# Performance work log

Measured on AMD Instinct MI355X. Metric: run time of the kernel, lower is better.

Reference implementation:

```python
import jax, jax.numpy as jnp
import numpy as np

N_NODES = 100000
N_EDGES = 600000
D_FEAT = 128
HID = 128


def setup_inputs() -> dict:
    key = jax.random.key(0)
    ks = jax.random.split(key, 8)
    zi = jax.random.normal(ks[0], (N_NODES, D_FEAT), dtype=jnp.float32)
    zj = jax.random.normal(ks[1], (N_NODES, D_FEAT), dtype=jnp.float32)
    src = jax.random.randint(ks[2], (N_EDGES,), 0, N_NODES, dtype=jnp.int64 if jax.config.jax_enable_x64 else jnp.int32)
    dst = jax.random.randint(ks[3], (N_EDGES,), 0, N_NODES, dtype=jnp.int64 if jax.config.jax_enable_x64 else jnp.int32)
    W1 = jax.random.normal(ks[4], (2 * D_FEAT, HID), dtype=jnp.float32) * (1.0 / np.sqrt(2 * D_FEAT))
    b1 = jnp.zeros((HID,), dtype=jnp.float32)
    W3 = jax.random.normal(ks[5], (HID, 1), dtype=jnp.float32) * (1.0 / np.sqrt(HID))
    b3 = jnp.zeros((1,), dtype=jnp.float32)
    return {"zi": zi, "zj": zj, "src": src, "dst": dst,
            "W1": W1, "b1": b1, "W3": W3, "b3": b3}


def reference(zi, zj, src, dst, W1, b1, W3, b3):
    # Irregular gather: per-edge src/dst node features, then concat -> [E, 2*d]
    hi = zi[src]              # [E, d]
    hj = zj[dst]              # [E, d]
    raw = jnp.concatenate([hi, hj], axis=1)  # [E, 2d]
    # LR_Classification with n_layers=2: only linear_1 and linear_3 run
    # (the linear_2 loop executes n_layers-2 = 0 times); dropout is identity (eval).
    hid = jax.nn.relu(raw @ W1 + b1)          # [E, HID]
    logit = hid @ W3 + b3                     # [E, 1]
    return jax.nn.sigmoid(logit)
```

## Files before the change

kernel.cpp:

```cpp
#include <hip/hip_runtime.h>
#include <hip/hip_bf16.h>

typedef __attribute__((ext_vector_type(8))) short short8;
typedef __attribute__((ext_vector_type(4))) float f32x4;
typedef __attribute__((ext_vector_type(4))) unsigned int u32x4;
typedef __attribute__((ext_vector_type(2))) unsigned int u32x2;

#define DFEAT 128
#define LDW 136

__device__ __forceinline__ unsigned short f2bf(float f) {
    unsigned int u = __float_as_uint(f);
    u += 0x7FFFu + ((u >> 16) & 1u);
    return (unsigned short)(u >> 16);
}
__device__ __forceinline__ unsigned int cvt2(float lo, float hi) {
    unsigned int r;
    asm("v_cvt_pk_bf16_f32 %0, %1, %2" : "=v"(r) : "v"(lo), "v"(hi));
    return r;
}
__device__ __forceinline__ float bf2f(unsigned int bits) {
    return __uint_as_float(bits << 16);
}

__global__ __launch_bounds__(256) void node_gemm(
    const float* __restrict__ zi, const float* __restrict__ zj,
    const float* __restrict__ W1, const float* __restrict__ b1,
    unsigned short* __restrict__ Aout, unsigned short* __restrict__ Bout,
    int nN)
{
    __shared__ unsigned short Wt[128][LDW];
    __shared__ float bias_lds[128];
    const int table = blockIdx.y;
    const float* __restrict__ z = table ? zj : zi;
    unsigned short* __restrict__ outp = table ? Bout : Aout;

    for (int idx = threadIdx.x; idx < 128 * 128; idx += 256) {
        int c = idx & 127, k = idx >> 7;
        Wt[c][k] = f2bf(W1[(size_t)(table * 128 + k) * DFEAT + c]);
    }
    if (threadIdx.x < 128) bias_lds[threadIdx.x] = table ? 0.f : b1[threadIdx.x];
    __syncthreads();

    const int lane = threadIdx.x & 63;
    const int l15  = lane & 15;
    const int kg   = lane >> 4;
    int wv = blockIdx.x * 4 + (threadIdx.x >> 6);
    int nw = gridDim.x * 4;
    int nStrips = (nN + 15) >> 4;

    float4 cur[8];
    int s = wv;
    if (s < nStrips) {
        int row = s * 16 + l15;
        const float* zr = z + (size_t)(row < nN ? row : nN - 1) * DFEAT + kg * 8;
#pragma unroll
        for (int kk = 0; kk < 4; ++kk) {
            cur[2 * kk]     = *(const float4*)(zr + kk * 32);
            cur[2 * kk + 1] = *(const float4*)(zr + kk * 32 + 4);
        }
    }

    while (s < nStrips) {
        short8 bf[4];
#pragma unroll
        for (int kk = 0; kk < 4; ++kk) {
            union { unsigned int u[4]; short8 s8; } cv;
            cv.u[0] = cvt2(cur[2 * kk].x,     cur[2 * kk].y);
            cv.u[1] = cvt2(cur[2 * kk].z,     cur[2 * kk].w);
            cv.u[2] = cvt2(cur[2 * kk + 1].x, cur[2 * kk + 1].y);
            cv.u[3] = cvt2(cur[2 * kk + 1].z, cur[2 * kk + 1].w);
            bf[kk] = cv.s8;
        }

        int snext = s + nw;
        if (snext < nStrips) {
            int row = snext * 16 + l15;
            const float* zr = z + (size_t)(row < nN ? row : nN - 1) * DFEAT + kg * 8;
#pragma unroll
            for (int kk = 0; kk < 4; ++kk) {
                cur[2 * kk]     = *(const float4*)(zr + kk * 32);
                cur[2 * kk + 1] = *(const float4*)(zr + kk * 32 + 4);
            }
        }

        int row = s * 16 + l15;
        unsigned short* op = outp + (size_t)row * DFEAT + kg * 4;
#pragma unroll
        for (int h = 0; h < 2; ++h) {
            f32x4 acc[4];
#pragma unroll
            for (int ci = 0; ci < 4; ++ci)
                acc[ci] = *(const f32x4*)&bias_lds[(h * 4 + ci) * 16 + kg * 4];
#pragma unroll
            for (int kk = 0; kk < 4; ++kk) {
#pragma unroll
                for (int ci = 0; ci < 4; ++ci) {
                    short8 a = *(const short8*)&Wt[(h * 4 + ci) * 16 + l15][kk * 32 + kg * 8];
                    acc[ci] = __builtin_amdgcn_mfma_f32_16x16x32_bf16(a, bf[kk], acc[ci], 0, 0, 0);
                }
            }
            if (row < nN) {
#pragma unroll
                for (int ci = 0; ci < 4; ++ci) {
                    u32x2 v;
                    v[0] = cvt2(acc[ci][0], acc[ci][1]);
                    v[1] = cvt2(acc[ci][2], acc[ci][3]);
                    *(u32x2*)(op + (h * 4 + ci) * 16) = v;
                }
            }
        }
        s = snext;
    }
}

__global__ __launch_bounds__(256) void edge_kernel(
    const unsigned short* __restrict__ A, const unsigned short* __restrict__ B,
    const int* __restrict__ src, const int* __restrict__ dst,
    const float* __restrict__ W3, const float* __restrict__ b3,
    float* __restrict__ out, int nE)
{
    const int lane = threadIdx.x & 63;
    const int sub  = lane & 15;
    const int grp  = lane >> 4;

    float w3v[8];
#pragma unroll
    for (int j = 0; j < 8; ++j) w3v[j] = W3[sub * 8 + j];
    const float bb = b3[0];

    int wv = blockIdx.x * 4 + (threadIdx.x >> 6);
    int nw = gridDim.x * 4;

    for (int base = wv * 8; base < nE; base += nw * 8) {
        int e0 = base + grp;
        int e1 = base + 4 + grp;
        bool v0 = e0 < nE, v1 = e1 < nE;
        int s0 = v0 ? src[e0] : 0, d0 = v0 ? dst[e0] : 0;
        int s1 = v1 ? src[e1] : 0, d1 = v1 ? dst[e1] : 0;

        const u32x4* pa0 = (const u32x4*)(A + (size_t)s0 * DFEAT + sub * 8);
        const u32x4* pb0 = (const u32x4*)(B + (size_t)d0 * DFEAT + sub * 8);
        const u32x4* pa1 = (const u32x4*)(A + (size_t)s1 * DFEAT + sub * 8);
        const u32x4* pb1 = (const u32x4*)(B + (size_t)d1 * DFEAT + sub * 8);
        u32x4 av0 = *pa0, bv0 = *pb0;
        u32x4 av1 = *pa1, bv1 = *pb1;

        float p0 = 0.f, p1 = 0.f;
#pragma unroll
        for (int w = 0; w < 4; ++w) {
            float x0 = fmaxf(bf2f(av0[w] & 0xFFFFu) + bf2f(bv0[w] & 0xFFFFu), 0.f);
            float x1 = fmaxf(bf2f(av0[w] >> 16)     + bf2f(bv0[w] >> 16),     0.f);
            p0 = fmaf(x0, w3v[w * 2], p0);
            p0 = fmaf(x1, w3v[w * 2 + 1], p0);
            float y0 = fmaxf(bf2f(av1[w] & 0xFFFFu) + bf2f(bv1[w] & 0xFFFFu), 0.f);
            float y1 = fmaxf(bf2f(av1[w] >> 16)     + bf2f(bv1[w] >> 16),     0.f);
            p1 = fmaf(y0, w3v[w * 2], p1);
            p1 = fmaf(y1, w3v[w * 2 + 1], p1);
        }
#pragma unroll
        for (int off = 8; off > 0; off >>= 1) {
            p0 += __shfl_xor(p0, off, 64);
            p1 += __shfl_xor(p1, off, 64);
        }
        if (sub == 0) {
            if (v0) out[e0] = 1.f / (1.f + __expf(-(p0 + bb)));
            if (v1) out[e1] = 1.f / (1.f + __expf(-(p1 + bb)));
        }
    }
}

__global__ __launch_bounds__(256) void fallback_kernel(
    const float* __restrict__ zi, const float* __restrict__ zj,
    const int* __restrict__ src, const int* __restrict__ dst,
    const float* __restrict__ W1, const float* __restrict__ b1,
    const float* __restrict__ W3, const float* __restrict__ b3,
    float* __restrict__ out, int nE)
{
    int e = blockIdx.x * blockDim.x + threadIdx.x;
    if (e >= nE) return;
    const float* a = zi + (size_t)src[e] * DFEAT;
    const float* b = zj + (size_t)dst[e] * DFEAT;
    float logit = b3[0];
    for (int h = 0; h < 128; ++h) {
        float acc = b1[h];
        for (int k = 0; k < 128; ++k) acc = fmaf(a[k], W1[(size_t)k * 128 + h], acc);
        for (int k = 0; k < 128; ++k) acc = fmaf(b[k], W1[(size_t)(128 + k) * 128 + h], acc);
        if (acc > 0.f) logit = fmaf(acc, W3[h], logit);
    }
    out[e] = 1.f / (1.f + __expf(-logit));
}

extern "C" void kernel_launch(void* const* d_in, const int* in_sizes, int n_in,
                              void* d_out, int out_size, void* d_ws, size_t ws_size,
                              hipStream_t stream) {
    const float* zi = (const float*)d_in[0];
    const float* zj = (const float*)d_in[1];
    const int*  src = (const int*)d_in[2];
    const int*  dst = (const int*)d_in[3];
    const float* W1 = (const float*)d_in[4];
    const float* b1 = (const float*)d_in[5];
    const float* W3 = (const float*)d_in[6];
    const float* b3 = (const float*)d_in[7];
    float* out = (float*)d_out;

    int nN = in_sizes[0] / DFEAT;
    int nE = in_sizes[2];
    size_t abytes = (size_t)nN * DFEAT * sizeof(unsigned short);

    if (ws_size >= 2 * abytes) {
        unsigned short* A = (unsigned short*)d_ws;
        unsigned short* B = A + (size_t)nN * DFEAT;
        dim3 g1(512, 2, 1);
        node_gemm<<<g1, 256, 0, stream>>>(zi, zj, W1, b1, A, B, nN);
        edge_kernel<<<2048, 256, 0, stream>>>(A, B, src, dst, W3, b3, out, nE);
    } else {
        fallback_kernel<<<(nE + 255) / 256, 256, 0, stream>>>(
            zi, zj, src, dst, W1, b1, W3, b3, out, nE);
    }
}
```

Baseline: 80.56 us.

## Double-buffer loads two iterations ahead in node GEMM and edge gather kernels

Both kernels now use two register buffers and issue the loads for iteration s+2 while computing iteration s. In the node GEMM this covers the strip loads; in the edge kernel it covers the index fetch and the gathered bf16 rows. Scheduling barriers keep the prefetch loads ahead of the compute. The edge grid also drops from 2048 to 1875 blocks, so each wave gets a whole number of 8-edge chunks. This hides more gather latency in exchange for higher register pressure, which may reduce occupancy.

```diff
diff --git a/kernel.cpp b/kernel.cpp
--- a/kernel.cpp
+++ b/kernel.cpp
@@ -21,6 +21,17 @@
 }
 __device__ __forceinline__ float bf2f(unsigned int bits) {
     return __uint_as_float(bits << 16);
+}
+
+__device__ __forceinline__ void load_strip(float4 (&buf)[8], const float* __restrict__ z,
+                                           int ss, int nN, int l15, int kg) {
+    int row = ss * 16 + l15;
+    const float* zr = z + (size_t)(row < nN ? row : nN - 1) * DFEAT + kg * 8;
+#pragma unroll
+    for (int kk = 0; kk < 4; ++kk) {
+        buf[2 * kk]     = *(const float4*)(zr + kk * 32);
+        buf[2 * kk + 1] = *(const float4*)(zr + kk * 32 + 4);
+    }
 }
 
 __global__ __launch_bounds__(256) void node_gemm(
@@ -45,46 +56,28 @@
     const int lane = threadIdx.x & 63;
     const int l15  = lane & 15;
     const int kg   = lane >> 4;
-    int wv = blockIdx.x * 4 + (threadIdx.x >> 6);
-    int nw = gridDim.x * 4;
-    int nStrips = (nN + 15) >> 4;
-
-    float4 cur[8];
-    int s = wv;
-    if (s < nStrips) {
-        int row = s * 16 + l15;
-        const float* zr = z + (size_t)(row < nN ? row : nN - 1) * DFEAT + kg * 8;
-#pragma unroll
-        for (int kk = 0; kk < 4; ++kk) {
-            cur[2 * kk]     = *(const float4*)(zr + kk * 32);
-            cur[2 * kk + 1] = *(const float4*)(zr + kk * 32 + 4);
-        }
-    }
-
-    while (s < nStrips) {
+    const int wv = blockIdx.x * 4 + (threadIdx.x >> 6);
+    const int nw = gridDim.x * 4;
+    const int nStrips = (nN + 15) >> 4;
+
+    float4 c0[8], c1[8];
+
+    auto process = [&](float4 (&buf)[8], int ss) {
         short8 bf[4];
 #pragma unroll
         for (int kk = 0; kk < 4; ++kk) {
             union { unsigned int u[4]; short8 s8; } cv;
-            cv.u[0] = cvt2(cur[2 * kk].x,     cur[2 * kk].y);
-            cv.u[1] = cvt2(cur[2 * kk].z,     cur[2 * kk].w);
-            cv.u[2] = cvt2(cur[2 * kk + 1].x, cur[2 * kk + 1].y);
-            cv.u[3] = cvt2(cur[2 * kk + 1].z, cur[2 * kk + 1].w);
+            cv.u[0] = cvt2(buf[2 * kk].x,     buf[2 * kk].y);
+            cv.u[1] = cvt2(buf[2 * kk].z,     buf[2 * kk].w);
+            cv.u[2] = cvt2(buf[2 * kk + 1].x, buf[2 * kk + 1].y);
+            cv.u[3] = cvt2(buf[2 * kk + 1].z, buf[2 * kk + 1].w);
             bf[kk] = cv.s8;
         }
-
-        int snext = s + nw;
-        if (snext < nStrips) {
-            int row = snext * 16 + l15;
-            const float* zr = z + (size_t)(row < nN ? row : nN - 1) * DFEAT + kg * 8;
-#pragma unroll
-            for (int kk = 0; kk < 4; ++kk) {
-                cur[2 * kk]     = *(const float4*)(zr + kk * 32);
-                cur[2 * kk + 1] = *(const float4*)(zr + kk * 32 + 4);
-            }
-        }
-
-        int row = s * 16 + l15;
+        int sp = ss + 2 * nw;
+        if (sp < nStrips) load_strip(buf, z, sp, nN, l15, kg);
+        __builtin_amdgcn_sched_barrier(0);
+
+        int row = ss * 16 + l15;
         unsigned short* op = outp + (size_t)row * DFEAT + kg * 4;
 #pragma unroll
         for (int h = 0; h < 2; ++h) {
@@ -110,7 +103,18 @@
                 }
             }
         }
-        s = snext;
+    };
+
+    int s = wv;
+    if (s < nStrips)      load_strip(c0, z, s, nN, l15, kg);
+    if (s + nw < nStrips) load_strip(c1, z, s + nw, nN, l15, kg);
+
+    while (s < nStrips) {
+        process(c0, s);
+        s += nw;
+        if (s >= nStrips) break;
+        process(c1, s);
+        s += nw;
     }
 }
 
@@ -129,23 +133,15 @@
     for (int j = 0; j < 8; ++j) w3v[j] = W3[sub * 8 + j];
     const float bb = b3[0];
 
-    int wv = blockIdx.x * 4 + (threadIdx.x >> 6);
-    int nw = gridDim.x * 4;
-
-    for (int base = wv * 8; base < nE; base += nw * 8) {
-        int e0 = base + grp;
-        int e1 = base + 4 + grp;
-        bool v0 = e0 < nE, v1 = e1 < nE;
-        int s0 = v0 ? src[e0] : 0, d0 = v0 ? dst[e0] : 0;
-        int s1 = v1 ? src[e1] : 0, d1 = v1 ? dst[e1] : 0;
-
-        const u32x4* pa0 = (const u32x4*)(A + (size_t)s0 * DFEAT + sub * 8);
-        const u32x4* pb0 = (const u32x4*)(B + (size_t)d0 * DFEAT + sub * 8);
-        const u32x4* pa1 = (const u32x4*)(A + (size_t)s1 * DFEAT + sub * 8);
-        const u32x4* pb1 = (const u32x4*)(B + (size_t)d1 * DFEAT + sub * 8);
-        u32x4 av0 = *pa0, bv0 = *pb0;
-        u32x4 av1 = *pa1, bv1 = *pb1;
-
+    const int wv = blockIdx.x * 4 + (threadIdx.x >> 6);
+    const int nw = gridDim.x * 4;
+    const int nChunk = (nE + 7) >> 3;
+    const int nm1 = nE - 1;
+
+    int c = wv;
+    if (c >= nChunk) return;
+
+    auto compute = [&](u32x4 av0, u32x4 bv0, u32x4 av1, u32x4 bv1, int cc) {
         float p0 = 0.f, p1 = 0.f;
 #pragma unroll
         for (int w = 0; w < 4; ++w) {
@@ -164,9 +160,55 @@
             p1 += __shfl_xor(p1, off, 64);
         }
         if (sub == 0) {
-            if (v0) out[e0] = 1.f / (1.f + __expf(-(p0 + bb)));
-            if (v1) out[e1] = 1.f / (1.f + __expf(-(p1 + bb)));
-        }
+            int e0 = cc * 8 + grp, e1 = e0 + 4;
+            if (e0 < nE) out[e0] = 1.f / (1.f + __expf(-(p0 + bb)));
+            if (e1 < nE) out[e1] = 1.f / (1.f + __expf(-(p1 + bb)));
+        }
+    };
+
+    int e0 = c * 8 + grp, e1 = e0 + 4;
+    int i0 = e0 < nE ? e0 : nm1, i1 = e1 < nE ? e1 : nm1;
+    int sA0 = src[i0], dA0 = dst[i0], sA1 = src[i1], dA1 = dst[i1];
+    u32x4 avA0 = *(const u32x4*)(A + (size_t)sA0 * DFEAT + sub * 8);
+    u32x4 bvA0 = *(const u32x4*)(B + (size_t)dA0 * DFEAT + sub * 8);
+    u32x4 avA1 = *(const u32x4*)(A + (size_t)sA1 * DFEAT + sub * 8);
+    u32x4 bvA1 = *(const u32x4*)(B + (size_t)dA1 * DFEAT + sub * 8);
+
+    int cB = c + nw; if (cB >= nChunk) cB = nChunk - 1;
+    e0 = cB * 8 + grp; e1 = e0 + 4;
+    i0 = e0 < nE ? e0 : nm1; i1 = e1 < nE ? e1 : nm1;
+    int sB0 = src[i0], dB0 = dst[i0], sB1 = src[i1], dB1 = dst[i1];
+    u32x4 avB0 = *(const u32x4*)(A + (size_t)sB0 * DFEAT + sub * 8);
+    u32x4 bvB0 = *(const u32x4*)(B + (size_t)dB0 * DFEAT + sub * 8);
+    u32x4 avB1 = *(const u32x4*)(A + (size_t)sB1 * DFEAT + sub * 8);
+    u32x4 bvB1 = *(const u32x4*)(B + (size_t)dB1 * DFEAT + sub * 8);
+
+    while (true) {
+        int cp = c + 2 * nw; if (cp >= nChunk) cp = nChunk - 1;
+        e0 = cp * 8 + grp; e1 = e0 + 4;
+        i0 = e0 < nE ? e0 : nm1; i1 = e1 < nE ? e1 : nm1;
+        int sp0 = src[i0], dp0 = dst[i0], sp1 = src[i1], dp1 = dst[i1];
+        compute(avA0, bvA0, avA1, bvA1, c);
+        avA0 = *(const u32x4*)(A + (size_t)sp0 * DFEAT + sub * 8);
+        bvA0 = *(const u32x4*)(B + (size_t)dp0 * DFEAT + sub * 8);
+        avA1 = *(const u32x4*)(A + (size_t)sp1 * DFEAT + sub * 8);
+        bvA1 = *(const u32x4*)(B + (size_t)dp1 * DFEAT + sub * 8);
+        __builtin_amdgcn_sched_barrier(0);
+        c += nw;
+        if (c >= nChunk) break;
+
+        cp = c + 2 * nw; if (cp >= nChunk) cp = nChunk - 1;
+        e0 = cp * 8 + grp; e1 = e0 + 4;
+        i0 = e0 < nE ? e0 : nm1; i1 = e1 < nE ? e1 : nm1;
+        sp0 = src[i0]; dp0 = dst[i0]; sp1 = src[i1]; dp1 = dst[i1];
+        compute(avB0, bvB0, avB1, bvB1, c);
+        avB0 = *(const u32x4*)(A + (size_t)sp0 * DFEAT + sub * 8);
+        bvB0 = *(const u32x4*)(B + (size_t)dp0 * DFEAT + sub * 8);
+        avB1 = *(const u32x4*)(A + (size_t)sp1 * DFEAT + sub * 8);
+        bvB1 = *(const u32x4*)(B + (size_t)dp1 * DFEAT + sub * 8);
+        __builtin_amdgcn_sched_barrier(0);
+        c += nw;
+        if (c >= nChunk) break;
     }
 }
 
@@ -213,7 +255,7 @@
         unsigned short* B = A + (size_t)nN * DFEAT;
         dim3 g1(512, 2, 1);
         node_gemm<<<g1, 256, 0, stream>>>(zi, zj, W1, b1, A, B, nN);
-        edge_kernel<<<2048, 256, 0, stream>>>(A, B, src, dst, W3, b3, out, nE);
+        edge_kernel<<<1875, 256, 0, stream>>>(A, B, src, dst, W3, b3, out, nE);
     } else {
         fallback_kernel<<<(nE + 255) / 256, 256, 0, stream>>>(
             zi, zj, src, dst, W1, b1, W3, b3, out, nE);
```

Result: slower. 87.30 us (+8.4%).
